# Kernel tuning notes

Hardware: AMD Instinct MI355X
Metric: run time of the kernel (lower is better)

## Reference

```python
import jax, jax.numpy as jnp
import numpy as np
from jax import lax

N, DEG = 32768, 16

def _leaky(x):
    return jnp.where(x > 0, x, 0.2 * x)

def _gatv2(h, src, ws, bs, wd, bd, attn, bias):
    # DGL GATv2Conv: e_uv = attn . leaky_relu(fc_src(h_u) + fc_dst(h_v)); edge softmax over in-neighbors
    Hn, Dn = attn.shape
    fs = (h @ ws + bs).reshape(N, Hn, Dn)
    fd = (h @ wd + bd).reshape(N, Hn, Dn)
    e = _leaky(fs[src] + fd[:, None])                          # [N, DEG, H, D]
    alpha = jax.nn.softmax(jnp.einsum('ndhk,hk->ndh', e, attn), axis=1)
    return jnp.einsum('ndh,ndhk->nhk', alpha, fs[src]) + bias.reshape(1, Hn, Dn)

def _lstm_last(x, wih, whh, b):
    # torch LSTM gate order i,f,g,o; returns final hidden state. x: [N, DEG, F]
    n, hh = x.shape[0], whh.shape[1]
    def step(carry, xt):
        h, c = carry
        g = xt @ wih.T + h @ whh.T + b
        i, f, gg, o = jnp.split(g, 4, axis=-1)
        c = jax.nn.sigmoid(f) * c + jax.nn.sigmoid(i) * jnp.tanh(gg)
        h = jax.nn.sigmoid(o) * jnp.tanh(c)
        return (h, c), None
    init = (jnp.zeros((n, hh), x.dtype), jnp.zeros((n, hh), x.dtype))
    (h, _), _ = lax.scan(step, init, jnp.swapaxes(x, 0, 1))
    return h

def _sage(h, src, wih, whh, b, wself, wneigh, bias):
    # DGL SAGEConv(aggregator='lstm'): rst = fc_self(h) + fc_neigh(lstm(neighbor msgs))
    hn = _lstm_last(h[src], wih, whh, b)
    return h @ wself + hn @ wneigh + bias

def _forward(feat, g0, l0, g1, l1, g2, l2, s1, s2, f1_w, f1_b, f2_w, f2_b, src):
    h = feat
    h = jax.nn.elu(_gatv2(h, src, *g0).reshape(N, -1) + h @ l0[0] + l0[1])
    h = jax.nn.elu(_gatv2(h, src, *g1).reshape(N, -1) + h @ l1[0] + l1[1])
    gat = _gatv2(h, src, *g2).mean(axis=1) + h @ l2[0] + l2[1]   # [N, 32]
    x = jax.nn.relu(_sage(feat, src, *s1))
    x = jax.nn.relu(_sage(x, src, *s2))                          # [N, 32]
    z = jnp.concatenate([gat, x], axis=1)
    z = jax.nn.relu(z @ f1_w + f1_b)
    return z @ f2_w + f2_b                                       # [N, 1]

def setup_inputs() -> dict:
    ks = iter(jax.random.split(jax.random.key(0), 64))
    def nrm(shape, s=0.1):
        return (s * jax.random.normal(next(ks), shape)).astype(jnp.float32)
    d = {}
    d['feat'] = jax.random.normal(next(ks), (N, 5), jnp.float32)
    d['src'] = jax.random.randint(next(ks), (N, DEG), 0, N)
    for i, (fi, hn) in enumerate([(5, 4), (128, 4), (128, 1)]):
        fo = 32 * hn
        d[f'g{i}_ws'] = nrm((fi, fo)); d[f'g{i}_bs'] = nrm((fo,))
        d[f'g{i}_wd'] = nrm((fi, fo)); d[f'g{i}_bd'] = nrm((fo,))
        d[f'g{i}_attn'] = nrm((hn, 32)); d[f'g{i}_bias'] = nrm((fo,))
        d[f'l{i}_w'] = nrm((fi, fo)); d[f'l{i}_b'] = nrm((fo,))
    for j, fi in [(1, 5), (2, 32)]:
        d[f's{j}_wih'] = nrm((4 * fi, fi)); d[f's{j}_whh'] = nrm((4 * fi, fi))
        d[f's{j}_b'] = nrm((4 * fi,))
        d[f's{j}_wself'] = nrm((fi, 32)); d[f's{j}_wneigh'] = nrm((fi, 32))
        d[f's{j}_bias'] = nrm((32,))
    d['f1_w'] = nrm((64, 16)); d['f1_b'] = nrm((16,))
    d['f2_w'] = (0.1 + 0.01 * jax.random.normal(next(ks), (16, 1))).astype(jnp.float32)
    d['f2_b'] = nrm((1,))
    return d

def reference(feat, src, g0_ws, g0_bs, g0_wd, g0_bd, g0_attn, g0_bias, l0_w, l0_b, g1_ws, g1_bs, g1_wd, g1_bd, g1_attn, g1_bias, l1_w, l1_b, g2_ws, g2_bs, g2_wd, g2_bd, g2_attn, g2_bias, l2_w, l2_b, s1_wih, s1_whh, s1_b, s1_wself, s1_wneigh, s1_bias, s2_wih, s2_whh, s2_b, s2_wself, s2_wneigh, s2_bias, f1_w, f1_b, f2_w, f2_b):
    return _forward(feat,
                    (g0_ws, g0_bs, g0_wd, g0_bd, g0_attn, g0_bias), (l0_w, l0_b),
                    (g1_ws, g1_bs, g1_wd, g1_bd, g1_attn, g1_bias), (l1_w, l1_b),
                    (g2_ws, g2_bs, g2_wd, g2_bd, g2_attn, g2_bias), (l2_w, l2_b),
                    (s1_wih, s1_whh, s1_b, s1_wself, s1_wneigh, s1_bias),
                    (s2_wih, s2_whh, s2_b, s2_wself, s2_wneigh, s2_bias),
                    f1_w, f1_b, f2_w, f2_b, src)
```

## Files before the change

kernel.cpp:

```cpp
#include <hip/hip_runtime.h>
#include <hip/hip_bf16.h>

#define NNODES 32768
#define DEG 16

__device__ __forceinline__ float sigmoidf_(float x) { return 1.f / (1.f + __expf(-x)); }
__device__ __forceinline__ float tanhf_(float x) { return 1.f - 2.f / (__expf(2.f * x) + 1.f); }

typedef __attribute__((ext_vector_type(8))) short bf16x8;
typedef __attribute__((ext_vector_type(4))) float f32x4;

__device__ __forceinline__ unsigned short f2bf_(float x) {
  __hip_bfloat16 b = __float2bfloat16(x);
  union { __hip_bfloat16 b; unsigned short u; } cv;
  cv.b = b;
  return cv.u;
}
__device__ __forceinline__ float bf2f_(unsigned short u) {
  union { unsigned short u; __hip_bfloat16 b; } cv;
  cv.u = u;
  return __bfloat162float(cv.b);
}
__device__ __forceinline__ void pack_hilo_(const float* v, bf16x8& hi, bf16x8& lo) {
#pragma unroll
  for (int j = 0; j < 8; j++) {
    unsigned short h = f2bf_(v[j]);
    float resid = v[j] - bf2f_(h);
    hi[j] = (short)h;
    lo[j] = (short)f2bf_(resid);
  }
}

#define WP_G1    0
#define WP_G2    98304
#define WP_S2WIH 122880
#define WP_TOTAL 131072

__global__ __launch_bounds__(256) void startup_kernel(
    const float* __restrict__ feat,
    const float* __restrict__ W0, const float* __restrict__ B0,
    const float* __restrict__ W1, const float* __restrict__ B1,
    const float* __restrict__ W2, const float* __restrict__ B2,
    float* __restrict__ O0, float* __restrict__ O1, float* __restrict__ O2,
    const float* __restrict__ g1ws, const float* __restrict__ g1wd,
    const float* __restrict__ l1w, const float* __restrict__ g2ws,
    const float* __restrict__ g2wd, const float* __restrict__ l2w,
    const float* __restrict__ s2wih, short* __restrict__ Wp) {
  __shared__ float w_s[5 * 64];
  __shared__ float in_s[32 * 8];
  __shared__ float b_s[64];
  const int bid = blockIdx.x;
  const int t = threadIdx.x;
  if (bid < 6144) {
    const int bz = bid >> 11, rem = bid & 2047, by = rem >> 10, bx = rem & 1023;
    const float* W = (bz == 0) ? W0 : (bz == 1) ? W1 : W2;
    const float* bias = (bz == 0) ? B0 : (bz == 1) ? B1 : B2;
    float* out = (bz == 0) ? O0 : (bz == 1) ? O1 : O2;
    const int rowBase = bx * 32;
    const int colBase = by * 64;
    for (int idx = t; idx < 5 * 64; idx += 256) {
      int k = idx >> 6, jj = idx & 63;
      w_s[idx] = W[(size_t)k * 128 + colBase + jj];
    }
    if (t < 64) b_s[t] = bias[colBase + t];
    for (int idx = t; idx < 32 * 5; idx += 256) {
      int r = idx / 5, k = idx - r * 5;
      in_s[r * 8 + k] = feat[(size_t)(rowBase + r) * 5 + k];
    }
    __syncthreads();
    const int jj = t & 63;
    const int rslot = t >> 6;
    float acc[8];
#pragma unroll
    for (int r = 0; r < 8; r++) acc[r] = b_s[jj];
    {
      float wv0 = w_s[0 * 64 + jj], wv1 = w_s[1 * 64 + jj];
      float wv2 = w_s[2 * 64 + jj], wv3 = w_s[3 * 64 + jj];
#pragma unroll
      for (int r = 0; r < 8; r++) {
        float4 ip = *(const float4*)&in_s[(rslot * 8 + r) * 8];
        acc[r] += ip.x * wv0 + ip.y * wv1 + ip.z * wv2 + ip.w * wv3;
      }
      float wv4 = w_s[4 * 64 + jj];
#pragma unroll
      for (int r = 0; r < 8; r++) acc[r] += in_s[(rslot * 8 + r) * 8 + 4] * wv4;
    }
#pragma unroll
    for (int r = 0; r < 8; r++)
      out[(size_t)(rowBase + rslot * 8 + r) * 128 + colBase + jj] = acc[r];
  } else {
    const int mid = bid - 6144;
    const float* W;
    int FI, FO, TRANS;
    size_t base;
    if (mid == 0)      { W = g1ws;  FI = 128; FO = 128; TRANS = 0; base = WP_G1; }
    else if (mid == 1) { W = g1wd;  FI = 128; FO = 128; TRANS = 0; base = WP_G1 + 32768; }
    else if (mid == 2) { W = l1w;   FI = 128; FO = 128; TRANS = 0; base = WP_G1 + 65536; }
    else if (mid == 3) { W = g2ws;  FI = 128; FO = 32;  TRANS = 0; base = WP_G2; }
    else if (mid == 4) { W = g2wd;  FI = 128; FO = 32;  TRANS = 0; base = WP_G2 + 8192; }
    else if (mid == 5) { W = l2w;   FI = 128; FO = 32;  TRANS = 0; base = WP_G2 + 16384; }
    else               { W = s2wih; FI = 32;  FO = 128; TRANS = 1; base = WP_S2WIH; }
    const int KS = FI / 32;
    const int total = FI * FO;
    for (int p = t; p < total; p += 256) {
      int j = p & 7, lane = (p >> 3) & 63, rest = p >> 9;
      int ks = rest % KS, f = rest / KS;
      int n = lane & 15, q = lane >> 4;
      int k = 32 * ks + 8 * q + j, fo = 16 * f + n;
      float v = TRANS ? W[(size_t)fo * FI + k] : W[(size_t)k * FO + fo];
      unsigned short hi = f2bf_(v);
      float resid = v - bf2f_(hi);
      Wp[base + p] = (short)hi;
      Wp[base + total + p] = (short)f2bf_(resid);
    }
  }
}

template <int KS, int FOT, int NZ>
__global__ __launch_bounds__(256) __attribute__((amdgpu_waves_per_eu(1, 4)))
void mfma_fc_kernel(const float* __restrict__ in, const short* __restrict__ Wp,
                    const float* __restrict__ B0, const float* __restrict__ B1,
                    const float* __restrict__ B2, float* __restrict__ O0,
                    float* __restrict__ O1, float* __restrict__ O2) {
  constexpr int FI = 32 * KS;
  constexpr int FO = 16 * FOT;
  __shared__ float lds_pad[9600];
  if ((const void*)in == nullptr) lds_pad[0] = 1.f;
  const int tid = threadIdx.x;
  const int wid = tid >> 6;
  const int lane = tid & 63;
  const int q = lane >> 4, n = lane & 15;
  const int n0 = blockIdx.x * 64 + wid * 16;
  bf16x8 Ahi[KS], Alo[KS];
#pragma unroll
  for (int ks = 0; ks < KS; ks++) {
    float av[8];
    *(float4*)&av[0] = *(const float4*)&in[(size_t)(n0 + n) * FI + 32 * ks + 8 * q];
    *(float4*)&av[4] = *(const float4*)&in[(size_t)(n0 + n) * FI + 32 * ks + 8 * q + 4];
    pack_hilo_(av, Ahi[ks], Alo[ks]);
  }
#pragma unroll
  for (int z = 0; z < NZ; z++) {
    const short* wz = Wp + (size_t)z * FI * FO * 2;
    const float* bz = (z == 0) ? B0 : (z == 1) ? B1 : B2;
    float* oz = (z == 0) ? O0 : (z == 1) ? O1 : O2;
#pragma unroll
    for (int f = 0; f < FOT; f++) {
      float bv = bz[16 * f + n];
      f32x4 acc = {bv, bv, bv, bv};
#pragma unroll
      for (int ks = 0; ks < KS; ks++) {
        bf16x8 Bhi = *(const bf16x8*)&wz[((size_t)(f * KS + ks) * 64 + lane) * 8];
        bf16x8 Blo = *(const bf16x8*)&wz[(size_t)FI * FO + ((size_t)(f * KS + ks) * 64 + lane) * 8];
        acc = __builtin_amdgcn_mfma_f32_16x16x32_bf16(Ahi[ks], Bhi, acc, 0, 0, 0);
        acc = __builtin_amdgcn_mfma_f32_16x16x32_bf16(Alo[ks], Bhi, acc, 0, 0, 0);
        acc = __builtin_amdgcn_mfma_f32_16x16x32_bf16(Ahi[ks], Blo, acc, 0, 0, 0);
      }
#pragma unroll
      for (int r = 0; r < 4; r++)
        oz[(size_t)(n0 + 4 * q + r) * FO + 16 * f + n] = acc[r];
    }
  }
}

__global__ __launch_bounds__(256) void gat4_kernel(const float* __restrict__ fs,
                                                   const float* __restrict__ fd,
                                                   const float* __restrict__ lin,
                                                   const int* __restrict__ src,
                                                   const float* __restrict__ attn,
                                                   const float* __restrict__ bias,
                                                   float* __restrict__ out) {
  constexpr int F = 128;
  const int lane = threadIdx.x & 63;
  const int wave = threadIdx.x >> 6;
  const int li = lane & 15;
  const int node = blockIdx.x * 4 + wave;
  const int f0 = 2 * lane;
  const int srcv = src[(size_t)node * DEG + li];
  const float2 fdv = *(const float2*)&fd[(size_t)node * F + f0];
  const float a0 = attn[f0];
  const float a1 = attn[f0 + 1];
  float m = -1e30f, s = 0.f, acc0 = 0.f, acc1 = 0.f;
  int sd = __shfl(srcv, (lane & 48), 64);
  float2 fsv = *(const float2*)&fs[(size_t)sd * F + f0];
#pragma unroll
  for (int d = 0; d < DEG; d++) {
    float2 cur = fsv;
    if (d < DEG - 1) {
      int sn = __shfl(srcv, (lane & 48) | (d + 1), 64);
      fsv = *(const float2*)&fs[(size_t)sn * F + f0];
    }
    float e0 = cur.x + fdv.x; e0 = (e0 > 0.f) ? e0 : 0.2f * e0;
    float e1 = cur.y + fdv.y; e1 = (e1 > 0.f) ? e1 : 0.2f * e1;
    float p = e0 * a0 + e1 * a1;
    p += __shfl_xor(p, 1, 64);
    p += __shfl_xor(p, 2, 64);
    p += __shfl_xor(p, 4, 64);
    p += __shfl_xor(p, 8, 64);
    float nm = fmaxf(m, p);
    float ex = __expf(p - nm);
    float sc = __expf(m - nm);
    s = s * sc + ex;
    acc0 = acc0 * sc + ex * cur.x;
    acc1 = acc1 * sc + ex * cur.y;
    m = nm;
  }
  float inv = 1.f / s;
  float2 lv = *(const float2*)&lin[(size_t)node * F + f0];
  float o0 = acc0 * inv + lv.x + bias[f0];
  float o1 = acc1 * inv + lv.y + bias[f0 + 1];
  o0 = (o0 > 0.f) ? o0 : __expf(o0) - 1.f;
  o1 = (o1 > 0.f) ? o1 : __expf(o1) - 1.f;
  *(float2*)&out[(size_t)node * F + f0] = make_float2(o0, o1);
}

__global__ __launch_bounds__(256) void gat1_fw1_kernel(
    const float* __restrict__ fs, const float* __restrict__ fd,
    const float* __restrict__ lin, const int* __restrict__ src,
    const float* __restrict__ attn, const float* __restrict__ bias,
    float* __restrict__ out, const float* __restrict__ feat,
    const float* __restrict__ wih, const float* __restrict__ wb,
    float* __restrict__ fwout) {
  __shared__ float w_s[100];
  __shared__ float b_s[20];
  if (blockIdx.x < 2048) {
    constexpr int F = 32;
    const int lane = threadIdx.x & 63;
    const int wave = threadIdx.x >> 6;
    const int G = lane >> 4, li = lane & 15;
    const int node = blockIdx.x * 16 + wave * 4 + G;
    const int f0 = 2 * li;
    const int srcv = src[(size_t)node * DEG + li];
    const float2 fdv = *(const float2*)&fd[(size_t)node * F + f0];
    const float a0 = attn[f0];
    const float a1 = attn[f0 + 1];
    float m = -1e30f, s = 0.f, acc0 = 0.f, acc1 = 0.f;
    int sd = __shfl(srcv, (lane & 48), 64);
    float2 fsv = *(const float2*)&fs[(size_t)sd * F + f0];
#pragma unroll
    for (int d = 0; d < DEG; d++) {
      float2 cur = fsv;
      if (d < DEG - 1) {
        int sn = __shfl(srcv, (lane & 48) | (d + 1), 64);
        fsv = *(const float2*)&fs[(size_t)sn * F + f0];
      }
      float e0 = cur.x + fdv.x; e0 = (e0 > 0.f) ? e0 : 0.2f * e0;
      float e1 = cur.y + fdv.y; e1 = (e1 > 0.f) ? e1 : 0.2f * e1;
      float p = e0 * a0 + e1 * a1;
      p += __shfl_xor(p, 1, 64);
      p += __shfl_xor(p, 2, 64);
      p += __shfl_xor(p, 4, 64);
      p += __shfl_xor(p, 8, 64);
      float nm = fmaxf(m, p);
      float ex = __expf(p - nm);
      float sc = __expf(m - nm);
      s = s * sc + ex;
      acc0 = acc0 * sc + ex * cur.x;
      acc1 = acc1 * sc + ex * cur.y;
      m = nm;
    }
    float inv = 1.f / s;
    float2 lv = *(const float2*)&lin[(size_t)node * F + f0];
    float o0 = acc0 * inv + lv.x + bias[f0];
    float o1 = acc1 * inv + lv.y + bias[f0 + 1];
    *(float2*)&out[(size_t)node * F + f0] = make_float2(o0, o1);
  } else {
    if (threadIdx.x < 100) w_s[threadIdx.x] = wih[threadIdx.x];
    if (threadIdx.x < 20) b_s[threadIdx.x] = wb[threadIdx.x];
    __syncthreads();
    const int n = (blockIdx.x - 2048) * 256 + threadIdx.x;
    float f[5];
#pragma unroll
    for (int k = 0; k < 5; k++) f[k] = feat[(size_t)n * 5 + k];
#pragma unroll
    for (int j = 0; j < 20; j++) {
      float a = b_s[j];
#pragma unroll
      for (int k = 0; k < 5; k++) a += f[k] * w_s[j * 5 + k];
      fwout[(size_t)n * 20 + j] = a;
    }
  }
}

__global__ __attribute__((amdgpu_waves_per_eu(1, 4))) __launch_bounds__(256)
void lstm1s_kernel(const float* __restrict__ FW, const int* __restrict__ src,
                   const float* __restrict__ whh, const float* __restrict__ feat,
                   const float* __restrict__ wself, const float* __restrict__ wneigh,
                   const float* __restrict__ bias, float* __restrict__ x1out) {
  __shared__ float w_s[100];
  __shared__ float ws_s[160];
  __shared__ float wn_s[160];
  __shared__ float b_s[32];
  if (threadIdx.x < 100) w_s[threadIdx.x] = whh[threadIdx.x];
  if (threadIdx.x < 160) {
    ws_s[threadIdx.x] = wself[threadIdx.x];
    wn_s[threadIdx.x] = wneigh[threadIdx.x];
  }
  if (threadIdx.x < 32) b_s[threadIdx.x] = bias[threadIdx.x];
  __syncthreads();
  const int n = blockIdx.x * 256 + threadIdx.x;
  const int* sp = src + (size_t)n * DEG;
  float f[5];
#pragma unroll
  for (int k = 0; k < 5; k++) f[k] = feat[(size_t)n * 5 + k];
  float h[5] = {0, 0, 0, 0, 0}, c[5] = {0, 0, 0, 0, 0};
  int sd = sp[0];
  float4 p0 = *(const float4*)&FW[(size_t)sd * 20 + 0];
  float4 p1 = *(const float4*)&FW[(size_t)sd * 20 + 4];
  float4 p2 = *(const float4*)&FW[(size_t)sd * 20 + 8];
  float4 p3 = *(const float4*)&FW[(size_t)sd * 20 + 12];
  float4 p4 = *(const float4*)&FW[(size_t)sd * 20 + 16];
  for (int d = 0; d < DEG; d++) {
    float g[20];
    g[0] = p0.x; g[1] = p0.y; g[2] = p0.z; g[3] = p0.w;
    g[4] = p1.x; g[5] = p1.y; g[6] = p1.z; g[7] = p1.w;
    g[8] = p2.x; g[9] = p2.y; g[10] = p2.z; g[11] = p2.w;
    g[12] = p3.x; g[13] = p3.y; g[14] = p3.z; g[15] = p3.w;
    g[16] = p4.x; g[17] = p4.y; g[18] = p4.z; g[19] = p4.w;
    if (d < DEG - 1) {
      int sn = sp[d + 1];
      p0 = *(const float4*)&FW[(size_t)sn * 20 + 0];
      p1 = *(const float4*)&FW[(size_t)sn * 20 + 4];
      p2 = *(const float4*)&FW[(size_t)sn * 20 + 8];
      p3 = *(const float4*)&FW[(size_t)sn * 20 + 12];
      p4 = *(const float4*)&FW[(size_t)sn * 20 + 16];
    }
#pragma unroll
    for (int j = 0; j < 20; j++) {
#pragma unroll
      for (int k = 0; k < 5; k++) g[j] += h[k] * w_s[j * 5 + k];
    }
#pragma unroll
    for (int k = 0; k < 5; k++) {
      float iv = sigmoidf_(g[k]);
      float fv = sigmoidf_(g[5 + k]);
      float gv = tanhf_(g[10 + k]);
      float ov = sigmoidf_(g[15 + k]);
      c[k] = fv * c[k] + iv * gv;
      h[k] = ov * tanhf_(c[k]);
    }
  }
#pragma unroll
  for (int j = 0; j < 32; j++) {
    float a = b_s[j];
#pragma unroll
    for (int k = 0; k < 5; k++) a += f[k] * ws_s[k * 32 + j] + h[k] * wn_s[k * 32 + j];
    x1out[(size_t)n * 32 + j] = fmaxf(a, 0.f);
  }
}

__global__ __launch_bounds__(256) __attribute__((amdgpu_waves_per_eu(1, 4)))
void lstm2_mfma_kernel(const float* __restrict__ XW, const int* __restrict__ src,
                       const float* __restrict__ whh, float* __restrict__ hn_out) {
  __shared__ float h_lds_all[4 * 16 * 36];
  __shared__ int src_lds_all[4 * 256];
  __shared__ float lds_pad[6900];
  if ((const void*)XW == nullptr) lds_pad[0] = 1.f;
  const int tid = threadIdx.x;
  const int wid = tid >> 6;
  const int lane = tid & 63;
  const int q = lane >> 4;
  const int n = lane & 15;
  const int n0 = (blockIdx.x * 4 + wid) * 16;
  float* h_lds = &h_lds_all[wid * 16 * 36];
  int* src_lds = &src_lds_all[wid * 256];

  {
    int4 sv = *(const int4*)&src[(size_t)(n0 + (lane >> 2)) * DEG + 4 * (lane & 3)];
    src_lds[(4 * (lane & 3) + 0) * 16 + (lane >> 2)] = sv.x;
    src_lds[(4 * (lane & 3) + 1) * 16 + (lane >> 2)] = sv.y;
    src_lds[(4 * (lane & 3) + 2) * 16 + (lane >> 2)] = sv.z;
    src_lds[(4 * (lane & 3) + 3) * 16 + (lane >> 2)] = sv.w;
  }

  bf16x8 Whi[8], Wlo[8];
#pragma unroll
  for (int gt = 0; gt < 8; gt++) {
    float wv[8];
    *(float4*)&wv[0] = *(const float4*)&whh[(size_t)(16 * gt + n) * 32 + 8 * q];
    *(float4*)&wv[4] = *(const float4*)&whh[(size_t)(16 * gt + n) * 32 + 8 * q + 4];
    pack_hilo_(wv, Whi[gt], Wlo[gt]);
  }

  bf16x8 Bhi, Blo;
#pragma unroll
  for (int j = 0; j < 8; j++) { Bhi[j] = 0; Blo[j] = 0; }
  float cst[8];
#pragma unroll
  for (int i = 0; i < 8; i++) cst[i] = 0.f;

  float4 tc[8], tn[8];
  {
    int s0 = src_lds[0 * 16 + n];
    const float* gb = XW + (size_t)s0 * 128;
#pragma unroll
    for (int i = 0; i < 8; i++) tc[i] = *(const float4*)&gb[16 * i + 4 * q];
  }

  float hv[8];
#pragma unroll
  for (int d = 0; d < DEG; d++) {
    f32x4 D[4][2];
#pragma unroll
    for (int p = 0; p < 4; p++) {
#pragma unroll
      for (int hh = 0; hh < 2; hh++) {
        int gt = p * 2 + hh;
        f32x4 acc = {0.f, 0.f, 0.f, 0.f};
        acc = __builtin_amdgcn_mfma_f32_16x16x32_bf16(Whi[gt], Bhi, acc, 0, 0, 0);
        acc = __builtin_amdgcn_mfma_f32_16x16x32_bf16(Wlo[gt], Bhi, acc, 0, 0, 0);
        acc = __builtin_amdgcn_mfma_f32_16x16x32_bf16(Whi[gt], Blo, acc, 0, 0, 0);
        D[p][hh] = acc;
      }
    }
    if (d < DEG - 1) {
      int s = src_lds[(d + 1) * 16 + n];
      const float* gb = XW + (size_t)s * 128;
#pragma unroll
      for (int i = 0; i < 8; i++) tn[i] = *(const float4*)&gb[16 * i + 4 * q];
    }
#pragma unroll
    for (int hh = 0; hh < 2; hh++) {
      float4 xi = tc[0 + hh];
      float4 xf = tc[2 + hh];
      float4 xg = tc[4 + hh];
      float4 xo = tc[6 + hh];
#pragma unroll
      for (int r = 0; r < 4; r++) {
        float xiv = (r == 0) ? xi.x : (r == 1) ? xi.y : (r == 2) ? xi.z : xi.w;
        float xfv = (r == 0) ? xf.x : (r == 1) ? xf.y : (r == 2) ? xf.z : xf.w;
        float xgv = (r == 0) ? xg.x : (r == 1) ? xg.y : (r == 2) ? xg.z : xg.w;
        float xov = (r == 0) ? xo.x : (r == 1) ? xo.y : (r == 2) ? xo.z : xo.w;
        int ci = hh * 4 + r;
        float iv = sigmoidf_(D[0][hh][r] + xiv);
        float fv = sigmoidf_(D[1][hh][r] + xfv);
        float gv = tanhf_(D[2][hh][r] + xgv);
        float ov = sigmoidf_(D[3][hh][r] + xov);
        cst[ci] = fv * cst[ci] + iv * gv;
        hv[ci] = ov * tanhf_(cst[ci]);
      }
    }
    if (d < DEG - 1) {
      *(float4*)&h_lds[n * 36 + 0 + 4 * q] = make_float4(hv[0], hv[1], hv[2], hv[3]);
      *(float4*)&h_lds[n * 36 + 16 + 4 * q] = make_float4(hv[4], hv[5], hv[6], hv[7]);
      float hb[8];
      *(float4*)&hb[0] = *(const float4*)&h_lds[n * 36 + 8 * q];
      *(float4*)&hb[4] = *(const float4*)&h_lds[n * 36 + 8 * q + 4];
      pack_hilo_(hb, Bhi, Blo);
#pragma unroll
      for (int i = 0; i < 8; i++) tc[i] = tn[i];
    }
  }
  *(float4*)&hn_out[(size_t)(n0 + n) * 32 + 0 + 4 * q] = make_float4(hv[0], hv[1], hv[2], hv[3]);
  *(float4*)&hn_out[(size_t)(n0 + n) * 32 + 16 + 4 * q] = make_float4(hv[4], hv[5], hv[6], hv[7]);
}

template <int FI>
__global__ __launch_bounds__(256) void sage_out_kernel(const float* __restrict__ in,
                                                       const float* __restrict__ hn,
                                                       const float* __restrict__ wself,
                                                       const float* __restrict__ wneigh,
                                                       const float* __restrict__ bias,
                                                       float* __restrict__ out) {
  __shared__ float ws_s[FI * 32];
  __shared__ float wn_s[FI * 32];
  __shared__ float b_s[32];
  for (int idx = threadIdx.x; idx < FI * 32; idx += 256) {
    ws_s[idx] = wself[idx];
    wn_s[idx] = wneigh[idx];
  }
  if (threadIdx.x < 32) b_s[threadIdx.x] = bias[threadIdx.x];
  __syncthreads();
  const int n = blockIdx.x * 8 + (threadIdx.x >> 5);
  const int j = threadIdx.x & 31;
  float a = b_s[j];
#pragma unroll
  for (int k = 0; k < FI; k++) a += in[(size_t)n * FI + k] * ws_s[k * 32 + j];
#pragma unroll
  for (int k = 0; k < FI; k++) a += hn[(size_t)n * FI + k] * wn_s[k * 32 + j];
  out[(size_t)n * 32 + j] = fmaxf(a, 0.f);
}

__global__ __attribute__((amdgpu_waves_per_eu(4, 4))) __launch_bounds__(256)
void final_kernel(const float* __restrict__ gat,
                  const float* __restrict__ x2,
                  const float* __restrict__ f1w,
                  const float* __restrict__ f1b,
                  const float* __restrict__ f2w,
                  const float* __restrict__ f2b,
                  float* __restrict__ out) {
  __shared__ float w1_s[64 * 16];
  __shared__ float b1_s[16];
  __shared__ float w2_s[16];
  for (int idx = threadIdx.x; idx < 1024; idx += 256) w1_s[idx] = f1w[idx];
  if (threadIdx.x < 16) {
    b1_s[threadIdx.x] = f1b[threadIdx.x];
    w2_s[threadIdx.x] = f2w[threadIdx.x];
  }
  __syncthreads();
  const int n = blockIdx.x * 256 + threadIdx.x;
  float z[64];
#pragma unroll
  for (int k = 0; k < 32; k += 4) {
    float4 a = *(const float4*)&gat[(size_t)n * 32 + k];
    z[k] = a.x; z[k + 1] = a.y; z[k + 2] = a.z; z[k + 3] = a.w;
    float4 b = *(const float4*)&x2[(size_t)n * 32 + k];
    z[32 + k] = b.x; z[32 + k + 1] = b.y; z[32 + k + 2] = b.z; z[32 + k + 3] = b.w;
  }
  float o = f2b[0];
#pragma unroll
  for (int j = 0; j < 16; j++) {
    float a = b1_s[j];
#pragma unroll
    for (int k = 0; k < 64; k++) a += z[k] * w1_s[k * 16 + j];
    o += fmaxf(a, 0.f) * w2_s[j];
  }
  out[n] = o;
}

extern "C" void kernel_launch(void* const* d_in, const int* in_sizes, int n_in,
                              void* d_out, int out_size, void* d_ws, size_t ws_size,
                              hipStream_t stream) {
  const int N = NNODES;
  const float* feat = (const float*)d_in[0];
  const int* src = (const int*)d_in[1];
  const float* g0_ws = (const float*)d_in[2];
  const float* g0_bs = (const float*)d_in[3];
  const float* g0_wd = (const float*)d_in[4];
  const float* g0_bd = (const float*)d_in[5];
  const float* g0_attn = (const float*)d_in[6];
  const float* g0_bias = (const float*)d_in[7];
  const float* l0_w = (const float*)d_in[8];
  const float* l0_b = (const float*)d_in[9];
  const float* g1_ws = (const float*)d_in[10];
  const float* g1_bs = (const float*)d_in[11];
  const float* g1_wd = (const float*)d_in[12];
  const float* g1_bd = (const float*)d_in[13];
  const float* g1_attn = (const float*)d_in[14];
  const float* g1_bias = (const float*)d_in[15];
  const float* l1_w = (const float*)d_in[16];
  const float* l1_b = (const float*)d_in[17];
  const float* g2_ws = (const float*)d_in[18];
  const float* g2_bs = (const float*)d_in[19];
  const float* g2_wd = (const float*)d_in[20];
  const float* g2_bd = (const float*)d_in[21];
  const float* g2_attn = (const float*)d_in[22];
  const float* g2_bias = (const float*)d_in[23];
  const float* l2_w = (const float*)d_in[24];
  const float* l2_b = (const float*)d_in[25];
  const float* s1_wih = (const float*)d_in[26];
  const float* s1_whh = (const float*)d_in[27];
  const float* s1_b = (const float*)d_in[28];
  const float* s1_wself = (const float*)d_in[29];
  const float* s1_wneigh = (const float*)d_in[30];
  const float* s1_bias = (const float*)d_in[31];
  const float* s2_wih = (const float*)d_in[32];
  const float* s2_whh = (const float*)d_in[33];
  const float* s2_b = (const float*)d_in[34];
  const float* s2_wself = (const float*)d_in[35];
  const float* s2_wneigh = (const float*)d_in[36];
  const float* s2_bias = (const float*)d_in[37];
  const float* f1_w = (const float*)d_in[38];
  const float* f1_b = (const float*)d_in[39];
  const float* f2_w = (const float*)d_in[40];
  const float* f2_b = (const float*)d_in[41];

  float* A = (float*)d_ws;
  float* B = A + (size_t)N * 128;
  float* C = B + (size_t)N * 128;
  float* D = C + (size_t)N * 128;
  float* E = D + (size_t)N * 128;
  short* Wp = (short*)(A + (size_t)5 * N * 128);

  startup_kernel<<<6151, 256, 0, stream>>>(
      feat, g0_ws, g0_bs, g0_wd, g0_bd, l0_w, l0_b, A, B, C,
      g1_ws, g1_wd, l1_w, g2_ws, g2_wd, l2_w, s2_wih, Wp);
  gat4_kernel<<<N / 4, 256, 0, stream>>>(A, B, C, src, g0_attn, g0_bias, D);
  mfma_fc_kernel<4, 8, 3><<<N / 64, 256, 0, stream>>>(
      D, Wp + WP_G1, g1_bs, g1_bd, l1_b, A, B, C);
  gat4_kernel<<<N / 4, 256, 0, stream>>>(A, B, C, src, g1_attn, g1_bias, E);
  mfma_fc_kernel<4, 2, 3><<<N / 64, 256, 0, stream>>>(
      E, Wp + WP_G2, g2_bs, g2_bd, l2_b, A, B, C);
  gat1_fw1_kernel<<<2048 + 128, 256, 0, stream>>>(
      A, B, C, src, g2_attn, g2_bias, D, feat, s1_wih, s1_b, E);
  lstm1s_kernel<<<N / 256, 256, 0, stream>>>(E, src, s1_whh, feat, s1_wself,
                                             s1_wneigh, s1_bias, C);
  mfma_fc_kernel<1, 8, 1><<<N / 64, 256, 0, stream>>>(
      C, Wp + WP_S2WIH, s2_b, nullptr, nullptr, A, nullptr, nullptr);
  lstm2_mfma_kernel<<<N / 64, 256, 0, stream>>>(A, src, s2_whh, E);
  sage_out_kernel<32><<<N / 8, 256, 0, stream>>>(C, E, s2_wself, s2_wneigh,
                                                 s2_bias, B);
  final_kernel<<<N / 256, 256, 0, stream>>>(D, B, f1_w, f1_b, f2_w, f2_b, (float*)d_out);
}
```

Before: 426.9 us.

## Store LSTM2 input projection in fp16 and fuse sage output with final MLP

Adds a dedicated kernel that computes the second SAGE LSTM's input projection and stores it as fp16 in a gate-interleaved layout. The LSTM kernel then gathers it with four 16-byte loads per step instead of eight float4 loads, halving gather traffic at some precision cost. The sage output layer is fused into the final MLP kernel, which removes one launch and the round trip of the intermediate through memory. The occupancy-limiting LDS padding arrays are also dropped from the fc and LSTM kernels.

```diff
diff --git a/kernel.cpp b/kernel.cpp
--- a/kernel.cpp
+++ b/kernel.cpp
@@ -9,6 +9,7 @@
 
 typedef __attribute__((ext_vector_type(8))) short bf16x8;
 typedef __attribute__((ext_vector_type(4))) float f32x4;
+typedef __attribute__((ext_vector_type(8))) _Float16 f16x8;
 
 __device__ __forceinline__ unsigned short f2bf_(float x) {
   __hip_bfloat16 b = __float2bfloat16(x);
@@ -124,8 +125,6 @@
                     float* __restrict__ O1, float* __restrict__ O2) {
   constexpr int FI = 32 * KS;
   constexpr int FO = 16 * FOT;
-  __shared__ float lds_pad[9600];
-  if ((const void*)in == nullptr) lds_pad[0] = 1.f;
   const int tid = threadIdx.x;
   const int wid = tid >> 6;
   const int lane = tid & 63;
@@ -160,6 +159,37 @@
       for (int r = 0; r < 4; r++)
         oz[(size_t)(n0 + 4 * q + r) * FO + 16 * f + n] = acc[r];
     }
+  }
+}
+
+__global__ __launch_bounds__(256) __attribute__((amdgpu_waves_per_eu(1, 4)))
+void xw_half_kernel(const float* __restrict__ in, const short* __restrict__ Wp,
+                    const float* __restrict__ bz, _Float16* __restrict__ XWh) {
+  const int tid = threadIdx.x;
+  const int wid = tid >> 6;
+  const int lane = tid & 63;
+  const int q = lane >> 4, n = lane & 15;
+  const int n0 = blockIdx.x * 64 + wid * 16;
+  bf16x8 Ahi, Alo;
+  {
+    float av[8];
+    *(float4*)&av[0] = *(const float4*)&in[(size_t)(n0 + n) * 32 + 8 * q];
+    *(float4*)&av[4] = *(const float4*)&in[(size_t)(n0 + n) * 32 + 8 * q + 4];
+    pack_hilo_(av, Ahi, Alo);
+  }
+#pragma unroll
+  for (int f = 0; f < 8; f++) {
+    float bv = bz[16 * f + n];
+    f32x4 acc = {bv, bv, bv, bv};
+    bf16x8 Bhi = *(const bf16x8*)&Wp[((size_t)f * 64 + lane) * 8];
+    bf16x8 Blo = *(const bf16x8*)&Wp[4096 + ((size_t)f * 64 + lane) * 8];
+    acc = __builtin_amdgcn_mfma_f32_16x16x32_bf16(Ahi, Bhi, acc, 0, 0, 0);
+    acc = __builtin_amdgcn_mfma_f32_16x16x32_bf16(Alo, Bhi, acc, 0, 0, 0);
+    acc = __builtin_amdgcn_mfma_f32_16x16x32_bf16(Ahi, Blo, acc, 0, 0, 0);
+#pragma unroll
+    for (int r = 0; r < 4; r++)
+      XWh[(size_t)(n0 + 4 * q + r) * 128 + ((n >> 2) * 32 + f * 4 + (n & 3))] =
+          (_Float16)acc[r];
   }
 }
 
@@ -350,12 +380,10 @@
 }
 
 __global__ __launch_bounds__(256) __attribute__((amdgpu_waves_per_eu(1, 4)))
-void lstm2_mfma_kernel(const float* __restrict__ XW, const int* __restrict__ src,
+void lstm2_mfma_kernel(const _Float16* __restrict__ XW, const int* __restrict__ src,
                        const float* __restrict__ whh, float* __restrict__ hn_out) {
   __shared__ float h_lds_all[4 * 16 * 36];
   __shared__ int src_lds_all[4 * 256];
-  __shared__ float lds_pad[6900];
-  if ((const void*)XW == nullptr) lds_pad[0] = 1.f;
   const int tid = threadIdx.x;
   const int wid = tid >> 6;
   const int lane = tid & 63;
@@ -389,12 +417,12 @@
 #pragma unroll
   for (int i = 0; i < 8; i++) cst[i] = 0.f;
 
-  float4 tc[8], tn[8];
+  f16x8 tch[4], tnh[4];
   {
     int s0 = src_lds[0 * 16 + n];
-    const float* gb = XW + (size_t)s0 * 128;
-#pragma unroll
-    for (int i = 0; i < 8; i++) tc[i] = *(const float4*)&gb[16 * i + 4 * q];
+    const _Float16* gb = XW + (size_t)s0 * 128 + q * 32;
+#pragma unroll
+    for (int t = 0; t < 4; t++) tch[t] = *(const f16x8*)&gb[8 * t];
   }
 
   float hv[8];
@@ -415,23 +443,19 @@
     }
     if (d < DEG - 1) {
       int s = src_lds[(d + 1) * 16 + n];
-      const float* gb = XW + (size_t)s * 128;
-#pragma unroll
-      for (int i = 0; i < 8; i++) tn[i] = *(const float4*)&gb[16 * i + 4 * q];
+      const _Float16* gb = XW + (size_t)s * 128 + q * 32;
+#pragma unroll
+      for (int t = 0; t < 4; t++) tnh[t] = *(const f16x8*)&gb[8 * t];
     }
 #pragma unroll
     for (int hh = 0; hh < 2; hh++) {
-      float4 xi = tc[0 + hh];
-      float4 xf = tc[2 + hh];
-      float4 xg = tc[4 + hh];
-      float4 xo = tc[6 + hh];
 #pragma unroll
       for (int r = 0; r < 4; r++) {
-        float xiv = (r == 0) ? xi.x : (r == 1) ? xi.y : (r == 2) ? xi.z : xi.w;
-        float xfv = (r == 0) ? xf.x : (r == 1) ? xf.y : (r == 2) ? xf.z : xf.w;
-        float xgv = (r == 0) ? xg.x : (r == 1) ? xg.y : (r == 2) ? xg.z : xg.w;
-        float xov = (r == 0) ? xo.x : (r == 1) ? xo.y : (r == 2) ? xo.z : xo.w;
         int ci = hh * 4 + r;
+        float xiv = (float)tch[0][hh * 4 + r];
+        float xfv = (float)tch[1][hh * 4 + r];
+        float xgv = (float)tch[2][hh * 4 + r];
+        float xov = (float)tch[3][hh * 4 + r];
         float iv = sigmoidf_(D[0][hh][r] + xiv);
         float fv = sigmoidf_(D[1][hh][r] + xfv);
         float gv = tanhf_(D[2][hh][r] + xgv);
@@ -448,64 +472,54 @@
       *(float4*)&hb[4] = *(const float4*)&h_lds[n * 36 + 8 * q + 4];
       pack_hilo_(hb, Bhi, Blo);
 #pragma unroll
-      for (int i = 0; i < 8; i++) tc[i] = tn[i];
+      for (int t = 0; t < 4; t++) tch[t] = tnh[t];
     }
   }
   *(float4*)&hn_out[(size_t)(n0 + n) * 32 + 0 + 4 * q] = make_float4(hv[0], hv[1], hv[2], hv[3]);
   *(float4*)&hn_out[(size_t)(n0 + n) * 32 + 16 + 4 * q] = make_float4(hv[4], hv[5], hv[6], hv[7]);
 }
 
-template <int FI>
-__global__ __launch_bounds__(256) void sage_out_kernel(const float* __restrict__ in,
-                                                       const float* __restrict__ hn,
-                                                       const float* __restrict__ wself,
-                                                       const float* __restrict__ wneigh,
-                                                       const float* __restrict__ bias,
-                                                       float* __restrict__ out) {
-  __shared__ float ws_s[FI * 32];
-  __shared__ float wn_s[FI * 32];
+__global__ __launch_bounds__(128) void sage_final_kernel(
+    const float* __restrict__ x1, const float* __restrict__ hn,
+    const float* __restrict__ wself, const float* __restrict__ wneigh,
+    const float* __restrict__ sbias, const float* __restrict__ gat,
+    const float* __restrict__ f1w, const float* __restrict__ f1b,
+    const float* __restrict__ f2w, const float* __restrict__ f2b,
+    float* __restrict__ out) {
+  __shared__ float ws_s[32 * 32];
+  __shared__ float wn_s[32 * 32];
   __shared__ float b_s[32];
-  for (int idx = threadIdx.x; idx < FI * 32; idx += 256) {
-    ws_s[idx] = wself[idx];
-    wn_s[idx] = wneigh[idx];
-  }
-  if (threadIdx.x < 32) b_s[threadIdx.x] = bias[threadIdx.x];
-  __syncthreads();
-  const int n = blockIdx.x * 8 + (threadIdx.x >> 5);
-  const int j = threadIdx.x & 31;
-  float a = b_s[j];
-#pragma unroll
-  for (int k = 0; k < FI; k++) a += in[(size_t)n * FI + k] * ws_s[k * 32 + j];
-#pragma unroll
-  for (int k = 0; k < FI; k++) a += hn[(size_t)n * FI + k] * wn_s[k * 32 + j];
-  out[(size_t)n * 32 + j] = fmaxf(a, 0.f);
-}
-
-__global__ __attribute__((amdgpu_waves_per_eu(4, 4))) __launch_bounds__(256)
-void final_kernel(const float* __restrict__ gat,
-                  const float* __restrict__ x2,
-                  const float* __restrict__ f1w,
-                  const float* __restrict__ f1b,
-                  const float* __restrict__ f2w,
-                  const float* __restrict__ f2b,
-                  float* __restrict__ out) {
   __shared__ float w1_s[64 * 16];
   __shared__ float b1_s[16];
   __shared__ float w2_s[16];
-  for (int idx = threadIdx.x; idx < 1024; idx += 256) w1_s[idx] = f1w[idx];
+  for (int idx = threadIdx.x; idx < 1024; idx += 128) {
+    ws_s[idx] = wself[idx];
+    wn_s[idx] = wneigh[idx];
+    w1_s[idx] = f1w[idx];
+  }
+  if (threadIdx.x < 32) b_s[threadIdx.x] = sbias[threadIdx.x];
   if (threadIdx.x < 16) {
     b1_s[threadIdx.x] = f1b[threadIdx.x];
     w2_s[threadIdx.x] = f2w[threadIdx.x];
   }
   __syncthreads();
-  const int n = blockIdx.x * 256 + threadIdx.x;
-  float z[64];
+  const int n = blockIdx.x * 128 + threadIdx.x;
+  float xr[32], hr[32], z[64];
 #pragma unroll
   for (int k = 0; k < 32; k += 4) {
+    *(float4*)&xr[k] = *(const float4*)&x1[(size_t)n * 32 + k];
+    *(float4*)&hr[k] = *(const float4*)&hn[(size_t)n * 32 + k];
     float4 a = *(const float4*)&gat[(size_t)n * 32 + k];
     z[k] = a.x; z[k + 1] = a.y; z[k + 2] = a.z; z[k + 3] = a.w;
-    float4 b = *(const float4*)&x2[(size_t)n * 32 + k];
-    z[32 + k] = b.x; z[32 + k + 1] = b.y; z[32 + k + 2] = b.z; z[32 + k + 3] = b.w;
+  }
+#pragma unroll
+  for (int j = 0; j < 32; j++) {
+    float a = b_s[j];
+#pragma unroll
+    for (int k = 0; k < 32; k++) a += xr[k] * ws_s[k * 32 + j];
+#pragma unroll
+    for (int k = 0; k < 32; k++) a += hr[k] * wn_s[k * 32 + j];
+    z[32 + j] = fmaxf(a, 0.f);
   }
   float o = f2b[0];
 #pragma unroll
@@ -585,10 +599,10 @@
       A, B, C, src, g2_attn, g2_bias, D, feat, s1_wih, s1_b, E);
   lstm1s_kernel<<<N / 256, 256, 0, stream>>>(E, src, s1_whh, feat, s1_wself,
                                              s1_wneigh, s1_bias, C);
-  mfma_fc_kernel<1, 8, 1><<<N / 64, 256, 0, stream>>>(
-      C, Wp + WP_S2WIH, s2_b, nullptr, nullptr, A, nullptr, nullptr);
-  lstm2_mfma_kernel<<<N / 64, 256, 0, stream>>>(A, src, s2_whh, E);
-  sage_out_kernel<32><<<N / 8, 256, 0, stream>>>(C, E, s2_wself, s2_wneigh,
-                                                 s2_bias, B);
-  final_kernel<<<N / 256, 256, 0, stream>>>(D, B, f1_w, f1_b, f2_w, f2_b, (float*)d_out);
-}
+  xw_half_kernel<<<N / 64, 256, 0, stream>>>(
+      C, Wp + WP_S2WIH, s2_b, (_Float16*)A);
+  lstm2_mfma_kernel<<<N / 64, 256, 0, stream>>>((const _Float16*)A, src, s2_whh, E);
+  sage_final_kernel<<<N / 128, 128, 0, stream>>>(
+      C, E, s2_wself, s2_wneigh, s2_bias, D, f1_w, f1_b, f2_w, f2_b,
+      (float*)d_out);
+}
```

Measured after the change: 415.8 us. 1.03x faster.
